# Performance work log

Hardware: AMD Instinct MI355X
Metric: run time of the kernel (lower is better)

The kernel has to match this reference:

```python
import jax, jax.numpy as jnp
import numpy as np

SCALE = 1.0  # std of the Normal error model (init arg `scale`)
B, P, D, T = 32, 256, 64, 4096


def setup_inputs() -> dict:
    key = jax.random.key(0)
    k1, k2, k3 = jax.random.split(key, 3)
    data = jax.random.normal(k1, (B, P, D), dtype=jnp.float32)
    targets = jax.random.normal(k2, (B, P), dtype=jnp.float32)
    task_pool = jax.random.normal(k3, (T, D, 1), dtype=jnp.float32)
    return {"data": data, "targets": targets, "task_pool": task_pool}


def reference(data, targets, task_pool):
    # W: (n_dims, n_tasks), matching task_pool.squeeze(-1).T in the original
    W = task_pool[..., 0].T
    dt = data.dtype

    # Per-point, per-task predictions and Gaussian log-likelihoods, computed ONCE.
    # The original recomputes X@W and the log-prob sum for every prefix i (O(n^2));
    # here a single cumsum over the point axis reproduces the same prefix sums.
    pred_per_task = jnp.einsum('bpd,dt->bpt', data, W)          # (B, P, T)
    err = targets[..., None] - pred_per_task                     # (B, P, T)
    log_norm = -jnp.log(jnp.asarray(SCALE, dt)) - 0.5 * jnp.log(jnp.asarray(2.0 * np.pi, dt))
    scores = -0.5 * (err / SCALE) ** 2 + log_norm                # Normal(0, scale).log_prob

    cum = jnp.cumsum(scores, axis=1)                             # cum[:, i] = sum_{j<=i}
    # Posterior for predicting point i uses points 0..i-1; point 0 uses a uniform
    # posterior (original: W.mean(dim=1) == softmax(zeros) @ W.T).
    log_lik = jnp.concatenate([jnp.zeros_like(cum[:, :1]), cum[:, :-1]], axis=1)
    post = jax.nn.softmax(log_lik, axis=-1)                      # (B, P, T)

    w_mmse = jnp.einsum('bpt,dt->bpd', post, W)                  # posterior-mean weights
    return jnp.einsum('bpd,bpd->bp', data, w_mmse)               # (B, P)
```

## Files before the change

### kernel.cpp

```cpp
#include <hip/hip_runtime.h>
#include <hip/hip_bf16.h>
#include <math.h>

#define Bb 32
#define Pp 256
#define Dd 64
#define Tt 4096

typedef unsigned short ushort_t;
typedef __attribute__((ext_vector_type(8))) short bf16x8;
typedef __attribute__((ext_vector_type(4))) float f32x4;

#define TRIP_BYTES ((size_t)Bb * Pp * 64 * 8)
#define A_BF_BYTES ((size_t)Bb * Pp * Dd * 2)
#define B_BF_BYTES ((size_t)Tt * Dd * 2)
#define WS_NEED    (TRIP_BYTES + 2 * A_BF_BYTES + 2 * B_BF_BYTES)

#define C2 (-0.7213475204444817f)

__device__ __forceinline__ float fexp2(float x) {
  float r; asm("v_exp_f32 %0, %1" : "=v"(r) : "v"(x)); return r;
}
__device__ __forceinline__ float flog2(float x) {
  float r; asm("v_log_f32 %0, %1" : "=v"(r) : "v"(x)); return r;
}
__device__ __forceinline__ float frcp(float x) {
  float r; asm("v_rcp_f32 %0, %1" : "=v"(r) : "v"(x)); return r;
}

template <int CTRL>
__device__ __forceinline__ float dppf(float x) {
  return __builtin_bit_cast(float,
      __builtin_amdgcn_update_dpp(0, __builtin_bit_cast(int, x), CTRL, 0xF, 0xF, true));
}

__device__ __forceinline__ f32x4 mfma6(bf16x8 ah0, bf16x8 ah1, bf16x8 al0, bf16x8 al1,
                                       bf16x8 bh0, bf16x8 bh1, bf16x8 bl0, bf16x8 bl1) {
  f32x4 a = (f32x4)0.f;
  a = __builtin_amdgcn_mfma_f32_16x16x32_bf16(ah0, bh0, a, 0, 0, 0);
  a = __builtin_amdgcn_mfma_f32_16x16x32_bf16(ah1, bh1, a, 0, 0, 0);
  a = __builtin_amdgcn_mfma_f32_16x16x32_bf16(ah0, bl0, a, 0, 0, 0);
  a = __builtin_amdgcn_mfma_f32_16x16x32_bf16(al0, bh0, a, 0, 0, 0);
  a = __builtin_amdgcn_mfma_f32_16x16x32_bf16(ah1, bl1, a, 0, 0, 0);
  a = __builtin_amdgcn_mfma_f32_16x16x32_bf16(al1, bh1, a, 0, 0, 0);
  return a;
}

__global__ __launch_bounds__(256) void k_conv(const float* __restrict__ data,
                                              const float* __restrict__ Wt,
                                              ushort_t* __restrict__ Ah, ushort_t* __restrict__ Al,
                                              ushort_t* __restrict__ Bh, ushort_t* __restrict__ Bl) {
  const int i  = blockIdx.x * 256 + threadIdx.x;
  const int NA = Bb * Pp * Dd;
  const float x = (i < NA) ? data[i] : Wt[i - NA];
  const __hip_bfloat16 h = __float2bfloat16(x);
  const float hf = __bfloat162float(h);
  const __hip_bfloat16 l = __float2bfloat16(x - hf);
  if (i < NA) { Ah[i] = *(const ushort_t*)&h; Al[i] = *(const ushort_t*)&l; }
  else        { const int j = i - NA;
                Bh[j] = *(const ushort_t*)&h; Bl[j] = *(const ushort_t*)&l; }
}

__global__ __launch_bounds__(256, 2) void k_main(const ushort_t* __restrict__ Ah,
                                                 const ushort_t* __restrict__ Al,
                                                 const ushort_t* __restrict__ Bh,
                                                 const ushort_t* __restrict__ Bl,
                                                 const float* __restrict__ targets,
                                                 float2* __restrict__ trips) {
  const int tid  = threadIdx.x;
  const int wid  = tid >> 6;
  const int lane = tid & 63;
  const int quad = lane >> 4;
  const int l16  = lane & 15;
  const int b     = blockIdx.x >> 4;
  const int strip = blockIdx.x & 15;
  const int t0    = strip * 256;
  const int wstrip = strip * 4 + wid;

  bf16x8 vbh0[4], vbh1[4], vbl0[4], vbl1[4];
#pragma unroll
  for (int nt = 0; nt < 4; ++nt) {
    const size_t boff = (size_t)(t0 + wid * 64 + nt * 16 + l16) * Dd + quad * 8;
    vbh0[nt] = *(const bf16x8*)(Bh + boff);
    vbh1[nt] = *(const bf16x8*)(Bh + boff + 32);
    vbl0[nt] = *(const bf16x8*)(Bl + boff);
    vbl1[nt] = *(const bf16x8*)(Bl + boff + 32);
  }

  const ushort_t* arow_base = Ah + (size_t)b * Pp * Dd;
  const ushort_t* alow_base = Al + (size_t)b * Pp * Dd;
  const float* tgt          = targets + b * Pp;
  float2* __restrict__ trb  = trips + (size_t)b * Pp * 64;

  float R[4];
#pragma unroll
  for (int nt = 0; nt < 4; ++nt) R[nt] = 0.f;

  const size_t aoff0 = (size_t)l16 * Dd + quad * 8;
  bf16x8 ah0 = *(const bf16x8*)(arow_base + aoff0);
  bf16x8 ah1 = *(const bf16x8*)(arow_base + aoff0 + 32);
  bf16x8 al0 = *(const bf16x8*)(alow_base + aoff0);
  bf16x8 al1 = *(const bf16x8*)(alow_base + aoff0 + 32);
  float4 tq  = *(const float4*)(tgt + quad * 4);

#pragma unroll 1
  for (int sg = 0; sg < 16; ++sg) {
    const int pn = ((sg + 1) & 15) * 16;
    const size_t an = (size_t)(pn + l16) * Dd + quad * 8;
    const bf16x8 nah0 = *(const bf16x8*)(arow_base + an);
    const bf16x8 nah1 = *(const bf16x8*)(arow_base + an + 32);
    const bf16x8 nal0 = *(const bf16x8*)(alow_base + an);
    const bf16x8 nal1 = *(const bf16x8*)(alow_base + an + 32);
    const float4 ntq  = *(const float4*)(tgt + pn + quad * 4);

    float cc[4][4], av[4][4];
#pragma unroll
    for (int nt = 0; nt < 4; ++nt) {
      const f32x4 a = mfma6(ah0, ah1, al0, al1,
                            vbh0[nt], vbh1[nt], vbl0[nt], vbl1[nt]);
      float sc0, sc1, sc2, sc3;
      { const float e = tq.x - a[0]; sc0 = C2 * e * e; }
      { const float e = tq.y - a[1]; sc1 = C2 * e * e; }
      { const float e = tq.z - a[2]; sc2 = C2 * e * e; }
      { const float e = tq.w - a[3]; sc3 = C2 * e * e; }

      const float colsum = (sc0 + sc1) + (sc2 + sc3);
      const float x1 = __shfl_xor(colsum, 16, 64);
      const float x2 = __shfl_xor(colsum, 32, 64);
      const float x3 = __shfl_xor(x1, 32, 64);
      const float pre = (quad == 0) ? 0.f
                      : (quad == 1) ? x1
                      : (quad == 2) ? (x2 + x3)
                                    : (x1 + x2 + x3);
      const float base = R[nt] + pre;
      cc[nt][0] = base;
      cc[nt][1] = base + sc0;
      cc[nt][2] = cc[nt][1] + sc1;
      cc[nt][3] = cc[nt][2] + sc2;
      av[nt][0] = a[0]; av[nt][1] = a[1]; av[nt][2] = a[2]; av[nt][3] = a[3];
      R[nt] += ((colsum + x1) + (x2 + x3));
    }

    float M[4];
#pragma unroll
    for (int r = 0; r < 4; ++r)
      M[r] = fmaxf(fmaxf(cc[0][r], cc[1][r]), fmaxf(cc[2][r], cc[3][r]));
#pragma unroll
    for (int r = 0; r < 4; ++r) M[r] = fmaxf(M[r], dppf<0xB1>(M[r]));
#pragma unroll
    for (int r = 0; r < 4; ++r) M[r] = fmaxf(M[r], dppf<0x4E>(M[r]));
#pragma unroll
    for (int r = 0; r < 4; ++r) M[r] = fmaxf(M[r], dppf<0x141>(M[r]));
#pragma unroll
    for (int r = 0; r < 4; ++r) M[r] = fmaxf(M[r], dppf<0x140>(M[r]));

    float ss[4], vv[4];
#pragma unroll
    for (int r = 0; r < 4; ++r) {
      float s = 0.f, v = 0.f;
#pragma unroll
      for (int nt = 0; nt < 4; ++nt) {
        const float e = fexp2(cc[nt][r] - M[r]);
        s += e;
        v = fmaf(e, av[nt][r], v);
      }
      ss[r] = s; vv[r] = v;
    }

#pragma unroll
    for (int r = 0; r < 4; ++r) { ss[r] += dppf<0xB1>(ss[r]);  vv[r] += dppf<0xB1>(vv[r]); }
#pragma unroll
    for (int r = 0; r < 4; ++r) { ss[r] += dppf<0x4E>(ss[r]);  vv[r] += dppf<0x4E>(vv[r]); }
#pragma unroll
    for (int r = 0; r < 4; ++r) { ss[r] += dppf<0x141>(ss[r]); vv[r] += dppf<0x141>(vv[r]); }
#pragma unroll
    for (int r = 0; r < 4; ++r) { ss[r] += dppf<0x140>(ss[r]); vv[r] += dppf<0x140>(vv[r]); }

    if (l16 == 0) {
#pragma unroll
      for (int r = 0; r < 4; ++r) {
        const float lm = M[r] + flog2(ss[r]);
        const float u  = vv[r] * frcp(ss[r]);
        const int p = sg * 16 + quad * 4 + r;
        trb[p * 64 + wstrip] = make_float2(lm, u);
      }
    }

    ah0 = nah0; ah1 = nah1; al0 = nal0; al1 = nal1; tq = ntq;
  }
}

__global__ __launch_bounds__(256) void k_merge(const float2* __restrict__ ws,
                                               float* __restrict__ out) {
  const int gt   = blockIdx.x * 256 + threadIdx.x;
  const int bp   = gt >> 6;
  const int lane = gt & 63;
  const float2 e = ws[(size_t)bp * 64 + lane];
  float M = e.x;
#pragma unroll
  for (int off = 32; off; off >>= 1) M = fmaxf(M, __shfl_xor(M, off, 64));
  const float f = fexp2(e.x - M);
  float S = f, V = f * e.y;
#pragma unroll
  for (int off = 32; off; off >>= 1) {
    S += __shfl_xor(S, off, 64);
    V += __shfl_xor(V, off, 64);
  }
  if (lane == 0) out[bp] = V / S;
}

__global__ __launch_bounds__(256) void k_scan_fused(const float* __restrict__ data,
                                                    const float* __restrict__ targets,
                                                    const float* __restrict__ task_pool,
                                                    float2* __restrict__ ws) {
  const int b     = blockIdx.x >> 4;
  const int wid   = threadIdx.x >> 6;
  const int lane  = threadIdx.x & 63;
  const int chunk = ((blockIdx.x & 15) << 2) | wid;
  const int t     = (chunk << 6) | lane;
  float w[Dd];
#pragma unroll
  for (int d = 0; d < Dd; d += 4) {
    const float4 r = *(const float4*)(task_pool + (size_t)t * Dd + d);
    w[d] = r.x; w[d + 1] = r.y; w[d + 2] = r.z; w[d + 3] = r.w;
  }
  const float* drow = data + (size_t)b * (Pp * Dd);
  const float* tgt  = targets + b * Pp;
  float2* wsb       = ws + (size_t)b * (Pp * 64);
  float c = 0.f;
  for (int p = 0; p < Pp; ++p) {
    float a0 = 0.f, a1 = 0.f, a2 = 0.f, a3 = 0.f;
    const float* r = drow + p * Dd;
#pragma unroll
    for (int d = 0; d < Dd; d += 4) {
      a0 = fmaf(r[d], w[d], a0);         a1 = fmaf(r[d + 1], w[d + 1], a1);
      a2 = fmaf(r[d + 2], w[d + 2], a2); a3 = fmaf(r[d + 3], w[d + 3], a3);
    }
    const float pred = (a0 + a1) + (a2 + a3);
    float m = c;
#pragma unroll
    for (int off = 32; off; off >>= 1) m = fmaxf(m, __shfl_xor(m, off, 64));
    const float e = fexp2(c - m);
    float s = e, v = e * pred;
#pragma unroll
    for (int off = 32; off; off >>= 1) {
      s += __shfl_xor(s, off, 64);
      v += __shfl_xor(v, off, 64);
    }
    if (lane == 0) wsb[p * 64 + chunk] = make_float2(m + flog2(s), v * frcp(s));
    const float err = tgt[p] - pred;
    c = fmaf(C2 * err, err, c);
  }
}

extern "C" void kernel_launch(void* const* d_in, const int* in_sizes, int n_in,
                              void* d_out, int out_size, void* d_ws, size_t ws_size,
                              hipStream_t stream) {
  const float* data      = (const float*)d_in[0];
  const float* targets   = (const float*)d_in[1];
  const float* task_pool = (const float*)d_in[2];
  float* out = (float*)d_out;

  if (ws_size >= WS_NEED) {
    float2*   trips = (float2*)d_ws;
    char*     cb    = (char*)d_ws + TRIP_BYTES;
    ushort_t* Ah    = (ushort_t*)cb;
    ushort_t* Al    = (ushort_t*)(cb + A_BF_BYTES);
    ushort_t* Bh    = (ushort_t*)(cb + 2 * A_BF_BYTES);
    ushort_t* Bl    = (ushort_t*)(cb + 2 * A_BF_BYTES + B_BF_BYTES);
    k_conv <<<dim3((Bb * Pp * Dd + Tt * Dd) / 256), dim3(256), 0, stream>>>(
        data, task_pool, Ah, Al, Bh, Bl);
    k_main <<<dim3(Bb * 16), dim3(256), 0, stream>>>(Ah, Al, Bh, Bl, targets, trips);
    k_merge<<<dim3((Bb * Pp * 64) / 256), dim3(256), 0, stream>>>(trips, out);
  } else {
    float2* trips = (float2*)d_ws;
    k_scan_fused<<<dim3(512), dim3(256), 0, stream>>>(data, targets, task_pool, trips);
    k_merge<<<dim3((Bb * Pp * 64) / 256), dim3(256), 0, stream>>>(trips, out);
  }
}
```

Measured before the change: 99.54 us.

## Software-pipeline MFMA score stage with softmax-reduction stage across point groups

Splits the per-group loop body into stage1 (A loads, MFMA products, local prefix scores) and stage2 (running-sum offset, max/exp/sum reductions, store). Stage1 for the next 16-point group is issued before stage2 of the current group, so MFMA and memory latency can overlap the DPP/exp reduction chain. The prefix offset R is now added after the fact, which removes the dependency between stages. The cost is more live registers for the double-buffered av/ccp arrays, which under launch_bounds(256,2) could cause spills.

```diff
diff --git a/kernel.cpp b/kernel.cpp
--- a/kernel.cpp
+++ b/kernel.cpp
@@ -59,6 +59,99 @@
   if (i < NA) { Ah[i] = *(const ushort_t*)&h; Al[i] = *(const ushort_t*)&l; }
   else        { const int j = i - NA;
                 Bh[j] = *(const ushort_t*)&h; Bl[j] = *(const ushort_t*)&l; }
+}
+
+__device__ __forceinline__ void stage1(
+    const ushort_t* __restrict__ arow_base, const ushort_t* __restrict__ alow_base,
+    size_t aoff, float4 tq, int quad,
+    const bf16x8 (&vbh0)[4], const bf16x8 (&vbh1)[4],
+    const bf16x8 (&vbl0)[4], const bf16x8 (&vbl1)[4],
+    float (&av)[4][4], float (&ccp)[4][4], float (&tot)[4]) {
+  const bf16x8 ah0 = *(const bf16x8*)(arow_base + aoff);
+  const bf16x8 ah1 = *(const bf16x8*)(arow_base + aoff + 32);
+  const bf16x8 al0 = *(const bf16x8*)(alow_base + aoff);
+  const bf16x8 al1 = *(const bf16x8*)(alow_base + aoff + 32);
+#pragma unroll
+  for (int nt = 0; nt < 4; ++nt) {
+    const f32x4 a = mfma6(ah0, ah1, al0, al1,
+                          vbh0[nt], vbh1[nt], vbl0[nt], vbl1[nt]);
+    float sc0, sc1, sc2, sc3;
+    { const float e = tq.x - a[0]; sc0 = C2 * e * e; }
+    { const float e = tq.y - a[1]; sc1 = C2 * e * e; }
+    { const float e = tq.z - a[2]; sc2 = C2 * e * e; }
+    { const float e = tq.w - a[3]; sc3 = C2 * e * e; }
+
+    const float colsum = (sc0 + sc1) + (sc2 + sc3);
+    const float x1 = __shfl_xor(colsum, 16, 64);
+    const float x2 = __shfl_xor(colsum, 32, 64);
+    const float x3 = __shfl_xor(x1, 32, 64);
+    const float pre = (quad == 0) ? 0.f
+                    : (quad == 1) ? x1
+                    : (quad == 2) ? (x2 + x3)
+                                  : (x1 + x2 + x3);
+    ccp[nt][0] = pre;
+    ccp[nt][1] = pre + sc0;
+    ccp[nt][2] = ccp[nt][1] + sc1;
+    ccp[nt][3] = ccp[nt][2] + sc2;
+    av[nt][0] = a[0]; av[nt][1] = a[1]; av[nt][2] = a[2]; av[nt][3] = a[3];
+    tot[nt] = ((colsum + x1) + (x2 + x3));
+  }
+}
+
+__device__ __forceinline__ void stage2(
+    int p0, int quad, int l16, int wstrip,
+    const float (&av)[4][4], const float (&ccp)[4][4], const float (&R)[4],
+    float2* __restrict__ trb) {
+  float cc[4][4];
+#pragma unroll
+  for (int nt = 0; nt < 4; ++nt)
+#pragma unroll
+    for (int r = 0; r < 4; ++r) cc[nt][r] = R[nt] + ccp[nt][r];
+
+  float M[4];
+#pragma unroll
+  for (int r = 0; r < 4; ++r)
+    M[r] = fmaxf(fmaxf(cc[0][r], cc[1][r]), fmaxf(cc[2][r], cc[3][r]));
+#pragma unroll
+  for (int r = 0; r < 4; ++r) M[r] = fmaxf(M[r], dppf<0xB1>(M[r]));
+#pragma unroll
+  for (int r = 0; r < 4; ++r) M[r] = fmaxf(M[r], dppf<0x4E>(M[r]));
+#pragma unroll
+  for (int r = 0; r < 4; ++r) M[r] = fmaxf(M[r], dppf<0x141>(M[r]));
+#pragma unroll
+  for (int r = 0; r < 4; ++r) M[r] = fmaxf(M[r], dppf<0x140>(M[r]));
+
+  float ss[4], vv[4];
+#pragma unroll
+  for (int r = 0; r < 4; ++r) {
+    float s = 0.f, v = 0.f;
+#pragma unroll
+    for (int nt = 0; nt < 4; ++nt) {
+      const float e = fexp2(cc[nt][r] - M[r]);
+      s += e;
+      v = fmaf(e, av[nt][r], v);
+    }
+    ss[r] = s; vv[r] = v;
+  }
+
+#pragma unroll
+  for (int r = 0; r < 4; ++r) { ss[r] += dppf<0xB1>(ss[r]);  vv[r] += dppf<0xB1>(vv[r]); }
+#pragma unroll
+  for (int r = 0; r < 4; ++r) { ss[r] += dppf<0x4E>(ss[r]);  vv[r] += dppf<0x4E>(vv[r]); }
+#pragma unroll
+  for (int r = 0; r < 4; ++r) { ss[r] += dppf<0x141>(ss[r]); vv[r] += dppf<0x141>(vv[r]); }
+#pragma unroll
+  for (int r = 0; r < 4; ++r) { ss[r] += dppf<0x140>(ss[r]); vv[r] += dppf<0x140>(vv[r]); }
+
+  if (l16 == 0) {
+#pragma unroll
+    for (int r = 0; r < 4; ++r) {
+      const float lm = M[r] + flog2(ss[r]);
+      const float u  = vv[r] * frcp(ss[r]);
+      const int p = p0 + quad * 4 + r;
+      trb[p * 64 + wstrip] = make_float2(lm, u);
+    }
+  }
 }
 
 __global__ __launch_bounds__(256, 2) void k_main(const ushort_t* __restrict__ Ah,
@@ -96,98 +189,35 @@
 #pragma unroll
   for (int nt = 0; nt < 4; ++nt) R[nt] = 0.f;
 
-  const size_t aoff0 = (size_t)l16 * Dd + quad * 8;
-  bf16x8 ah0 = *(const bf16x8*)(arow_base + aoff0);
-  bf16x8 ah1 = *(const bf16x8*)(arow_base + aoff0 + 32);
-  bf16x8 al0 = *(const bf16x8*)(alow_base + aoff0);
-  bf16x8 al1 = *(const bf16x8*)(alow_base + aoff0 + 32);
-  float4 tq  = *(const float4*)(tgt + quad * 4);
+  float avC[4][4], ccpC[4][4], totC[4];
+  {
+    const size_t aoff0 = (size_t)l16 * Dd + quad * 8;
+    const float4 tq0 = *(const float4*)(tgt + quad * 4);
+    stage1(arow_base, alow_base, aoff0, tq0, quad,
+           vbh0, vbh1, vbl0, vbl1, avC, ccpC, totC);
+  }
 
 #pragma unroll 1
-  for (int sg = 0; sg < 16; ++sg) {
-    const int pn = ((sg + 1) & 15) * 16;
+  for (int sg = 0; sg < 15; ++sg) {
+    float avN[4][4], ccpN[4][4], totN[4];
+    const int pn = (sg + 1) * 16;
     const size_t an = (size_t)(pn + l16) * Dd + quad * 8;
-    const bf16x8 nah0 = *(const bf16x8*)(arow_base + an);
-    const bf16x8 nah1 = *(const bf16x8*)(arow_base + an + 32);
-    const bf16x8 nal0 = *(const bf16x8*)(alow_base + an);
-    const bf16x8 nal1 = *(const bf16x8*)(alow_base + an + 32);
-    const float4 ntq  = *(const float4*)(tgt + pn + quad * 4);
-
-    float cc[4][4], av[4][4];
+    const float4 tqN = *(const float4*)(tgt + pn + quad * 4);
+    stage1(arow_base, alow_base, an, tqN, quad,
+           vbh0, vbh1, vbl0, vbl1, avN, ccpN, totN);
+
+    stage2(sg * 16, quad, l16, wstrip, avC, ccpC, R, trb);
+
 #pragma unroll
     for (int nt = 0; nt < 4; ++nt) {
-      const f32x4 a = mfma6(ah0, ah1, al0, al1,
-                            vbh0[nt], vbh1[nt], vbl0[nt], vbl1[nt]);
-      float sc0, sc1, sc2, sc3;
-      { const float e = tq.x - a[0]; sc0 = C2 * e * e; }
-      { const float e = tq.y - a[1]; sc1 = C2 * e * e; }
-      { const float e = tq.z - a[2]; sc2 = C2 * e * e; }
-      { const float e = tq.w - a[3]; sc3 = C2 * e * e; }
-
-      const float colsum = (sc0 + sc1) + (sc2 + sc3);
-      const float x1 = __shfl_xor(colsum, 16, 64);
-      const float x2 = __shfl_xor(colsum, 32, 64);
-      const float x3 = __shfl_xor(x1, 32, 64);
-      const float pre = (quad == 0) ? 0.f
-                      : (quad == 1) ? x1
-                      : (quad == 2) ? (x2 + x3)
-                                    : (x1 + x2 + x3);
-      const float base = R[nt] + pre;
-      cc[nt][0] = base;
-      cc[nt][1] = base + sc0;
-      cc[nt][2] = cc[nt][1] + sc1;
-      cc[nt][3] = cc[nt][2] + sc2;
-      av[nt][0] = a[0]; av[nt][1] = a[1]; av[nt][2] = a[2]; av[nt][3] = a[3];
-      R[nt] += ((colsum + x1) + (x2 + x3));
-    }
-
-    float M[4];
-#pragma unroll
-    for (int r = 0; r < 4; ++r)
-      M[r] = fmaxf(fmaxf(cc[0][r], cc[1][r]), fmaxf(cc[2][r], cc[3][r]));
-#pragma unroll
-    for (int r = 0; r < 4; ++r) M[r] = fmaxf(M[r], dppf<0xB1>(M[r]));
-#pragma unroll
-    for (int r = 0; r < 4; ++r) M[r] = fmaxf(M[r], dppf<0x4E>(M[r]));
-#pragma unroll
-    for (int r = 0; r < 4; ++r) M[r] = fmaxf(M[r], dppf<0x141>(M[r]));
-#pragma unroll
-    for (int r = 0; r < 4; ++r) M[r] = fmaxf(M[r], dppf<0x140>(M[r]));
-
-    float ss[4], vv[4];
-#pragma unroll
-    for (int r = 0; r < 4; ++r) {
-      float s = 0.f, v = 0.f;
-#pragma unroll
-      for (int nt = 0; nt < 4; ++nt) {
-        const float e = fexp2(cc[nt][r] - M[r]);
-        s += e;
-        v = fmaf(e, av[nt][r], v);
-      }
-      ss[r] = s; vv[r] = v;
-    }
-
-#pragma unroll
-    for (int r = 0; r < 4; ++r) { ss[r] += dppf<0xB1>(ss[r]);  vv[r] += dppf<0xB1>(vv[r]); }
-#pragma unroll
-    for (int r = 0; r < 4; ++r) { ss[r] += dppf<0x4E>(ss[r]);  vv[r] += dppf<0x4E>(vv[r]); }
-#pragma unroll
-    for (int r = 0; r < 4; ++r) { ss[r] += dppf<0x141>(ss[r]); vv[r] += dppf<0x141>(vv[r]); }
-#pragma unroll
-    for (int r = 0; r < 4; ++r) { ss[r] += dppf<0x140>(ss[r]); vv[r] += dppf<0x140>(vv[r]); }
-
-    if (l16 == 0) {
-#pragma unroll
-      for (int r = 0; r < 4; ++r) {
-        const float lm = M[r] + flog2(ss[r]);
-        const float u  = vv[r] * frcp(ss[r]);
-        const int p = sg * 16 + quad * 4 + r;
-        trb[p * 64 + wstrip] = make_float2(lm, u);
-      }
-    }
-
-    ah0 = nah0; ah1 = nah1; al0 = nal0; al1 = nal1; tq = ntq;
-  }
+      R[nt] += totC[nt];
+#pragma unroll
+      for (int r = 0; r < 4; ++r) { avC[nt][r] = avN[nt][r]; ccpC[nt][r] = ccpN[nt][r]; }
+      totC[nt] = totN[nt];
+    }
+  }
+
+  stage2(240, quad, l16, wstrip, avC, ccpC, R, trb);
 }
 
 __global__ __launch_bounds__(256) void k_merge(const float2* __restrict__ ws,
```

Result: no change. 99.54 us (-0.0%).
